# Kernel tuning notes

Measured on AMD Instinct MI355X. Metric: run time of the kernel, lower is better.

## Reference

```python
import jax, jax.numpy as jnp
import numpy as np

B, Cin, Cout, H, W = 4, 256, 256, 64, 64
DG, KH, KW = 2, 3, 3        # deformable_groups=2, kernel 3x3
K = KH * KW
CG = Cin // DG


def setup_inputs() -> dict:
    key = jax.random.key(0)
    ks = jax.random.split(key, 4)
    x = jax.random.normal(ks[0], (B, Cin, H, W), jnp.float32)
    # offset/mask-predicting 3x3 conv: 3*DG*K = 54 output channels
    # (small weights so sampled offsets stay in a realistic +-few-pixel range)
    w_off = jax.random.normal(ks[1], (3 * DG * K, Cin, KH, KW), jnp.float32) * 0.01
    b_off = jnp.zeros((3 * DG * K,), jnp.float32)
    weight = jax.random.normal(ks[2], (Cout, Cin, KH, KW), jnp.float32) * (1.0 / np.sqrt(Cin * K))
    bias = jnp.zeros((Cout,), jnp.float32)
    return {"x": x, "w_off": w_off, "b_off": b_off, "weight": weight, "bias": bias}


def _dcn_forward(x, w_off, b_off, weight, bias):
    # 1) predict offsets + modulation mask with a regular 3x3 conv
    om = jax.lax.conv_general_dilated(
        x, w_off, window_strides=(1, 1), padding=((1, 1), (1, 1)),
        dimension_numbers=('NCHW', 'OIHW', 'NCHW'))
    om = om + b_off[None, :, None, None]
    off = om[:, :2 * DG * K].reshape(B, DG, 2, K, H, W)        # [.,.,(dy,dx),k,h,w]
    mask = jax.nn.sigmoid(om[:, 2 * DG * K:]).reshape(B, DG, K, H, W)

    # 2) sampling positions: base grid (stride 1, pad 1, dilation 1) + learned offsets
    ky = jnp.repeat(jnp.arange(KH), KW).astype(jnp.float32)    # [K]
    kx = jnp.tile(jnp.arange(KW), KH).astype(jnp.float32)
    gy = jnp.arange(H, dtype=jnp.float32)
    gx = jnp.arange(W, dtype=jnp.float32)
    py = off[:, :, 0] + (gy[None, None, None, :, None] + ky[None, None, :, None, None] - 1.0)  # [B,DG,K,H,W]
    px = off[:, :, 1] + (gx[None, None, None, None, :] + kx[None, None, :, None, None] - 1.0)

    y0 = jnp.floor(py); x0 = jnp.floor(px)
    wy1 = py - y0; wx1 = px - x0
    wy0 = 1.0 - wy1; wx0 = 1.0 - wx1
    y0i = y0.astype(jnp.int32); x0i = x0.astype(jnp.int32)

    imgf = x.reshape(B, DG, CG, H * W)  # channel groups share their group's offsets

    def gather(iy, ix):
        # zero padding outside the image, as in the DCNv2 CUDA kernel
        valid = ((iy >= 0) & (iy < H) & (ix >= 0) & (ix < W)).astype(x.dtype)  # [B,DG,K,H,W]
        idx = jnp.clip(iy, 0, H - 1) * W + jnp.clip(ix, 0, W - 1)
        idx = idx.reshape(B, DG, K * H * W)
        v = jax.vmap(jax.vmap(lambda im, ii: im[:, ii]))(imgf, idx)  # [B,DG,CG,K*H*W]
        return v.reshape(B, DG, CG, K, H, W) * valid[:, :, None]

    # 3) bilinear interpolation of the 4 corners
    sampled = (gather(y0i,     x0i)     * (wy0 * wx0)[:, :, None]
             + gather(y0i,     x0i + 1) * (wy0 * wx1)[:, :, None]
             + gather(y0i + 1, x0i)     * (wy1 * wx0)[:, :, None]
             + gather(y0i + 1, x0i + 1) * (wy1 * wx1)[:, :, None])
    sampled = sampled * mask[:, :, None]  # modulation (DCNv2)

    # 4) weighted accumulation == grouped contraction over (channel, tap)
    wr = weight.reshape(Cout, DG, CG, K)
    out = jnp.einsum('odck,bdckhw->bohw', wr, sampled) + bias[None, :, None, None]
    return out


def reference(x, w_off, b_off, weight, bias):
    return _dcn_forward(x, w_off, b_off, weight, bias)
```

## Files before the change

### kernel.cpp

```cpp
#include <hip/hip_runtime.h>
#include <cstdint>

#define HW 4096

typedef __attribute__((ext_vector_type(8))) short bf16x8;
typedef __attribute__((ext_vector_type(4))) float f32x4;

__device__ __forceinline__ short f2bf(float f) {
    union { float f; uint32_t u; } v; v.f = f;
    uint32_t u = v.u;
    uint32_t r = (u + 0x7FFFu + ((u >> 16) & 1u)) >> 16;
    return (short)(r & 0xFFFFu);
}
__device__ __forceinline__ uint32_t cvtpk(float lo, float hi) {
    uint32_t r;
    asm("v_cvt_pk_bf16_f32 %0, %1, %2" : "=v"(r) : "v"(lo), "v"(hi));
    return r;
}
__device__ __forceinline__ float blo(uint32_t u) { return __uint_as_float(u << 16); }
__device__ __forceinline__ float bhi(uint32_t u) { return __uint_as_float(u & 0xFFFF0000u); }
__device__ __forceinline__ void glds16(const void* g, void* l) {
    __builtin_amdgcn_global_load_lds(
        (const __attribute__((address_space(1))) void*)g,
        (__attribute__((address_space(3))) void*)l, 16, 0, 0);
}

__global__ __launch_bounds__(256) void k_xt(
    const float* __restrict__ x, unsigned short* __restrict__ xT)
{
    __shared__ unsigned short s[64][65];
    const int t = threadIdx.x, lane = t & 63, grp = t >> 6;
    const int hw0 = blockIdx.x * 64, c0 = blockIdx.y * 64, b = blockIdx.z;
#pragma unroll
    for (int j = 0; j < 16; ++j) {
        int cc = grp * 16 + j;
        float v = x[((size_t)(b * 256 + c0 + cc)) * HW + hw0 + lane];
        s[cc][lane] = (unsigned short)f2bf(v);
    }
    __syncthreads();
#pragma unroll
    for (int j = 0; j < 16; ++j) {
        int hw2 = grp * 16 + j;
        xT[((size_t)b * HW + hw0 + hw2) * 256 + c0 + lane] = s[lane][hw2];
    }
}

__global__ __launch_bounds__(256) void k_wt2(
    const float* __restrict__ w_off, short* __restrict__ wTb)
{
    int e = blockIdx.x * 256 + threadIdx.x;
    int o = e / 2304, r = e - o * 2304;
    int tap = r >> 8, c = r & 255;
    wTb[e] = (o < 54) ? f2bf(w_off[(o * 256 + c) * 9 + tap]) : (short)0;
}

__global__ __launch_bounds__(256, 4) void k_omgemm(
    const short* __restrict__ wTb, const unsigned short* __restrict__ xT,
    float* __restrict__ om2p)
{
    __shared__ short As[2][64 * 32];
    __shared__ short Bs[2][64 * 32];
    const int t = threadIdx.x;
    const int wid = __builtin_amdgcn_readfirstlane(t >> 6);
    const int lane = t & 63, quad = lane >> 4, l16 = lane & 15;
    const int n0 = blockIdx.x * 64, b = n0 >> 12;
    const int ks = blockIdx.y;
    const int nr = t >> 2;
    const int ksh = (t & 3) * 8;
    const int px = (n0 + nr) & 4095, h = px >> 6, w = px & 63;
    const unsigned short* xb = xT + (size_t)b * HW * 256;
    const int cbase = ks * 18;

    auto loadB = [&](int c) -> uint4 {
        int tap = c >> 3, c0 = (c & 7) * 32;
        int hh = h + tap / 3 - 1, ww = w + tap % 3 - 1;
        uint4 bv = {0u, 0u, 0u, 0u};
        if (hh >= 0 && hh < 64 && ww >= 0 && ww < 64)
            bv = *(const uint4*)(xb + (size_t)(hh * 64 + ww) * 256 + c0 + ksh);
        return bv;
    };

    f32x4 acc[4];
#pragma unroll
    for (int i = 0; i < 4; ++i) acc[i] = (f32x4){0.f, 0.f, 0.f, 0.f};

    uint4 bv[2];
    bv[0] = loadB(cbase);
    glds16(wTb + (size_t)nr * 2304 + cbase * 32 + ksh, &As[0][t * 8]);
    *(uint4*)&Bs[0][t * 8] = bv[0];
    bv[1] = loadB(cbase + 1);

#pragma unroll 2
    for (int i = 0; i < 18; ++i) {
        const int p = i & 1;
        __syncthreads();
        if (i < 17) {
            glds16(wTb + (size_t)nr * 2304 + (cbase + i + 1) * 32 + ksh,
                   &As[1 - p][t * 8]);
            *(uint4*)&Bs[1 - p][t * 8] = bv[(i + 1) & 1];
        }
        if (i + 2 < 18) bv[i & 1] = loadB(cbase + i + 2);
        bf16x8 bf = *(const bf16x8*)&Bs[p][(wid * 16 + l16) * 32 + quad * 8];
#pragma unroll
        for (int mi = 0; mi < 4; ++mi) {
            bf16x8 af = *(const bf16x8*)&As[p][(mi * 16 + l16) * 32 + quad * 8];
            acc[mi] = __builtin_amdgcn_mfma_f32_16x16x32_bf16(af, bf, acc[mi], 0, 0, 0);
        }
    }
    const int n = n0 + wid * 16 + l16;
#pragma unroll
    for (int mi = 0; mi < 4; ++mi)
#pragma unroll
        for (int i = 0; i < 4; ++i)
            om2p[(size_t)(ks * 64 + mi * 16 + quad * 4 + i) * 16384 + n] = acc[mi][i];
}

__global__ __launch_bounds__(256) void k_wcvt2(
    const float* __restrict__ weight, short* __restrict__ a2)
{
    int e = blockIdx.x * 256 + threadIdx.x;
    int o = e / 2304, r = e - o * 2304;
    int dg = r / 1152, r2 = r - dg * 1152;
    int tap = r2 >> 7, c = r2 & 127;
    a2[e] = f2bf(weight[o * 2304 + (dg * 128 + c) * 9 + tap]);
}

__global__ __launch_bounds__(256) void k_plan(
    const float* __restrict__ om2p, const float* __restrict__ b_off,
    float4* __restrict__ planw, int4* __restrict__ plani)
{
    int e = blockIdx.x * 256 + threadIdx.x;
    int n = e & 16383, s = e >> 14;
    int dg = s >= 9 ? 1 : 0, tap = s - dg * 9;
    int h = (n >> 6) & 63, w = n & 63;
    int cdy = dg * 18 + tap, cdx = cdy + 9, cms = 36 + dg * 9 + tap;
    float dy = b_off[cdy], dx = b_off[cdx], ms = b_off[cms];
#pragma unroll
    for (int cs = 0; cs < 4; ++cs) {
        const float* p = om2p + (size_t)cs * 64 * 16384;
        dy += p[(size_t)cdy * 16384 + n];
        dx += p[(size_t)cdx * 16384 + n];
        ms += p[(size_t)cms * 16384 + n];
    }
    ms = 1.f / (1.f + __expf(-ms));
    float py = dy + (float)(h + tap / 3 - 1);
    float qx = dx + (float)(w + tap % 3 - 1);
    float y0f = floorf(py), x0f = floorf(qx);
    float wy1 = py - y0f, wx1 = qx - x0f;
    float wy0 = 1.f - wy1, wx0 = 1.f - wx1;
    int y0 = (int)y0f, x0 = (int)x0f;
    int y1 = y0 + 1, x1 = x0 + 1;
    bool vy0 = (y0 >= 0) & (y0 < 64), vy1 = (y1 >= 0) & (y1 < 64);
    bool vx0 = (x0 >= 0) & (x0 < 64), vx1 = (x1 >= 0) & (x1 < 64);
    int cy0 = min(max(y0, 0), 63), cy1 = min(max(y1, 0), 63);
    int cx0 = min(max(x0, 0), 63), cx1 = min(max(x1, 0), 63);
    float4 wv;
    wv.x = (vy0 && vx0) ? wy0 * wx0 * ms : 0.f;
    wv.y = (vy0 && vx1) ? wy0 * wx1 * ms : 0.f;
    wv.z = (vy1 && vx0) ? wy1 * wx0 * ms : 0.f;
    wv.w = (vy1 && vx1) ? wy1 * wx1 * ms : 0.f;
    int4 iv = make_int4((cy0 * 64 + cx0) << 9, (cy0 * 64 + cx1) << 9,
                        (cy1 * 64 + cx0) << 9, (cy1 * 64 + cx1) << 9);
    planw[e] = wv;
    plani[e] = iv;
}

__global__ __launch_bounds__(1024, 4) void k_fused(
    const short* __restrict__ A, const unsigned short* __restrict__ xT,
    const float4* __restrict__ planw, const int4* __restrict__ plani,
    const float* __restrict__ bias, float* __restrict__ out)
{
    __shared__ short As[2][4][256 * 32];
    __shared__ short Bs[2][4][64 * 32];
    const int t = threadIdx.x;
    const int wid = __builtin_amdgcn_readfirstlane(t >> 6);
    const int lane = t & 63;
    const int quad = lane >> 4, l16 = lane & 15;
    const int wr = wid & 7, wc = wid >> 3;

    const int lin = blockIdx.x;
    const int bn = ((lin & 7) << 5) | (lin >> 3);

    const int n0 = bn * 64, b = n0 >> 12;
    const char* xbb = (const char*)xT + (size_t)b * HW * 512;
    const int px = t >> 4;
    const int cc = (t >> 2) & 3;
    const int q8 = (t & 3) * 8;
    const int n = n0 + px;

    f32x4 acc[2][2];
#pragma unroll
    for (int i = 0; i < 2; ++i)
#pragma unroll
        for (int j = 0; j < 2; ++j) acc[i][j] = (f32x4){0.f, 0.f, 0.f, 0.f};

    float4 pw[2];
    int4 pi[2];
    uint4 g[2][4];

    auto planload = [&](int S) {
        pw[S & 1] = planw[(size_t)S * 16384 + n];
        pi[S & 1] = plani[(size_t)S * 16384 + n];
    };
    auto gather = [&](int j, uint4* gd) {
        const int cb = ((j >= 9 ? 128 : 0) + cc * 32 + q8) * 2;
        const int4 i4 = pi[j & 1];
        gd[0] = *(const uint4*)(xbb + i4.x + cb);
        gd[1] = *(const uint4*)(xbb + i4.y + cb);
        gd[2] = *(const uint4*)(xbb + i4.z + cb);
        gd[3] = *(const uint4*)(xbb + i4.w + cb);
    };
    const int arow = t >> 2;
    const int aq = t & 3;
    const int asw = (aq ^ ((arow >> 1) & 3)) * 8;
    auto stageA = [&](int j, int buf) {
#pragma unroll
        for (int ss = 0; ss < 4; ++ss)
            glds16(A + (size_t)arow * 2304 + (4 * j + ss) * 32 + asw,
                   &As[buf][ss][arow * 32 + aq * 8]);
    };
    const int bsw = ((t & 3) ^ ((px >> 1) & 3)) * 8;
    auto packwrite = [&](int j, int buf) {
        const float4 w4 = pw[j & 1];
        const uint4* gd = g[j & 1];
        float a0 = w4.x * blo(gd[0].x) + w4.y * blo(gd[1].x) + w4.z * blo(gd[2].x) + w4.w * blo(gd[3].x);
        float a1 = w4.x * bhi(gd[0].x) + w4.y * bhi(gd[1].x) + w4.z * bhi(gd[2].x) + w4.w * bhi(gd[3].x);
        float a2v = w4.x * blo(gd[0].y) + w4.y * blo(gd[1].y) + w4.z * blo(gd[2].y) + w4.w * blo(gd[3].y);
        float a3 = w4.x * bhi(gd[0].y) + w4.y * bhi(gd[1].y) + w4.z * bhi(gd[2].y) + w4.w * bhi(gd[3].y);
        float a4 = w4.x * blo(gd[0].z) + w4.y * blo(gd[1].z) + w4.z * blo(gd[2].z) + w4.w * blo(gd[3].z);
        float a5 = w4.x * bhi(gd[0].z) + w4.y * bhi(gd[1].z) + w4.z * bhi(gd[2].z) + w4.w * bhi(gd[3].z);
        float a6 = w4.x * blo(gd[0].w) + w4.y * blo(gd[1].w) + w4.z * blo(gd[2].w) + w4.w * blo(gd[3].w);
        float a7 = w4.x * bhi(gd[0].w) + w4.y * bhi(gd[1].w) + w4.z * bhi(gd[2].w) + w4.w * bhi(gd[3].w);
        uint4 o;
        o.x = cvtpk(a0, a1); o.y = cvtpk(a2v, a3);
        o.z = cvtpk(a4, a5); o.w = cvtpk(a6, a7);
        *(uint4*)&Bs[buf][cc][px * 32 + bsw] = o;
    };

    planload(0);
    gather(0, g[0]);
    stageA(0, 0);
    packwrite(0, 0);
    planload(1);
    gather(1, g[1]);

#pragma unroll 2
    for (int i = 0; i < 18; ++i) {
        const int p = i & 1;
        __syncthreads();
        if (i + 2 < 18) planload(i + 2);
        if (i < 17) {
            stageA(i + 1, 1 - p);
            packwrite(i + 1, 1 - p);
        }
        if (i + 2 < 18) gather(i + 2, g[i & 1]);
#pragma unroll
        for (int ss = 0; ss < 4; ++ss) {
            bf16x8 bfr[2];
#pragma unroll
            for (int ni = 0; ni < 2; ++ni) {
                const int row = wc * 32 + ni * 16 + l16;
                bfr[ni] = *(const bf16x8*)&Bs[p][ss][row * 32 + (quad ^ ((row >> 1) & 3)) * 8];
            }
#pragma unroll
            for (int mi = 0; mi < 2; ++mi) {
                const int row = wr * 32 + mi * 16 + l16;
                bf16x8 af = *(const bf16x8*)&As[p][ss][row * 32 + (quad ^ ((row >> 1) & 3)) * 8];
#pragma unroll
                for (int ni = 0; ni < 2; ++ni)
                    acc[mi][ni] = __builtin_amdgcn_mfma_f32_16x16x32_bf16(
                        af, bfr[ni], acc[mi][ni], 0, 0, 0);
            }
        }
    }

    const int m0 = wr * 32;
#pragma unroll
    for (int mi = 0; mi < 2; ++mi)
#pragma unroll
        for (int ni = 0; ni < 2; ++ni) {
            int nn = n0 + wc * 32 + ni * 16 + l16;
            int bidx = nn >> 12, hw = nn & 4095;
            float* op = out + (size_t)bidx * 256 * 4096 + hw;
#pragma unroll
            for (int r = 0; r < 4; ++r) {
                int m = m0 + mi * 16 + quad * 4 + r;
                op[(size_t)m * 4096] = acc[mi][ni][r] + bias[m];
            }
        }
}

extern "C" void kernel_launch(void* const* d_in, const int* in_sizes, int n_in,
                              void* d_out, int out_size, void* d_ws, size_t ws_size,
                              hipStream_t stream)
{
    const float* x      = (const float*)d_in[0];
    const float* w_off  = (const float*)d_in[1];
    const float* b_off  = (const float*)d_in[2];
    const float* weight = (const float*)d_in[3];
    const float* bias   = (const float*)d_in[4];
    float* out = (float*)d_out;
    char* ws = (char*)d_ws;

    unsigned short* xT   = (unsigned short*)(ws);
    short*          a2   = (short*)(ws + 8388608);
    short*          wTb  = (short*)(ws + 9568256);
    float4*         planw= (float4*)(ws + 9863168);
    int4*           plani= (int4*)(ws + 14581760);
    float*          om2p = (float*)d_out;

    hipLaunchKernelGGL(k_xt, dim3(64, 4, 4), dim3(256), 0, stream, x, xT);
    hipLaunchKernelGGL(k_wt2, dim3(576), dim3(256), 0, stream, w_off, wTb);
    hipLaunchKernelGGL(k_omgemm, dim3(256, 4), dim3(256), 0, stream, wTb, xT, om2p);
    hipLaunchKernelGGL(k_wcvt2, dim3(2304), dim3(256), 0, stream, weight, a2);
    hipLaunchKernelGGL(k_plan, dim3(1152), dim3(256), 0, stream, om2p, b_off, planw, plani);
    hipLaunchKernelGGL(k_fused, dim3(256), dim3(1024), 0, stream,
                       a2, xT, planw, plani, bias, out);
}
```

Measured before the change: 144.3 us.

## Merge weight conversion kernels and replace syncthreads with partial waitcnt barrier

Merges the two weight-conversion kernels into one launch, removing one kernel launch. In the fused gather-GEMM loop, __syncthreads is replaced by an explicit s_waitcnt vmcnt(4) plus s_barrier, with sched_barriers pinning the instruction order. Plan index loads are prefetched one stage further ahead, so gathers can stay in flight across the barrier. This relies on hand-counted outstanding memory operations, which is fragile: a wrong count gives a race.

After: 142.3 us. About the same (-1.4%).

```diff
diff --git a/kernel.cpp b/kernel.cpp
--- a/kernel.cpp
+++ b/kernel.cpp
@@ -45,13 +45,22 @@
     }
 }
 
-__global__ __launch_bounds__(256) void k_wt2(
-    const float* __restrict__ w_off, short* __restrict__ wTb)
+__global__ __launch_bounds__(256) void k_wcvt_all(
+    const float* __restrict__ weight, const float* __restrict__ w_off,
+    short* __restrict__ a2, short* __restrict__ wTb)
 {
     int e = blockIdx.x * 256 + threadIdx.x;
-    int o = e / 2304, r = e - o * 2304;
-    int tap = r >> 8, c = r & 255;
-    wTb[e] = (o < 54) ? f2bf(w_off[(o * 256 + c) * 9 + tap]) : (short)0;
+    if (e < 589824) {
+        int o = e / 2304, r = e - o * 2304;
+        int dg = r / 1152, r2 = r - dg * 1152;
+        int tap = r2 >> 7, c = r2 & 127;
+        a2[e] = f2bf(weight[o * 2304 + (dg * 128 + c) * 9 + tap]);
+    } else {
+        int e2 = e - 589824;
+        int o = e2 / 2304, r = e2 - o * 2304;
+        int tap = r >> 8, c = r & 255;
+        wTb[e2] = (o < 54) ? f2bf(w_off[(o * 256 + c) * 9 + tap]) : (short)0;
+    }
 }
 
 __global__ __launch_bounds__(256, 4) void k_omgemm(
@@ -113,16 +122,6 @@
 #pragma unroll
         for (int i = 0; i < 4; ++i)
             om2p[(size_t)(ks * 64 + mi * 16 + quad * 4 + i) * 16384 + n] = acc[mi][i];
-}
-
-__global__ __launch_bounds__(256) void k_wcvt2(
-    const float* __restrict__ weight, short* __restrict__ a2)
-{
-    int e = blockIdx.x * 256 + threadIdx.x;
-    int o = e / 2304, r = e - o * 2304;
-    int dg = r / 1152, r2 = r - dg * 1152;
-    int tap = r2 >> 7, c = r2 & 127;
-    a2[e] = f2bf(weight[o * 2304 + (dg * 128 + c) * 9 + tap]);
 }
 
 __global__ __launch_bounds__(256) void k_plan(
@@ -198,10 +197,8 @@
     int4 pi[2];
     uint4 g[2][4];
 
-    auto planload = [&](int S) {
-        pw[S & 1] = planw[(size_t)S * 16384 + n];
-        pi[S & 1] = plani[(size_t)S * 16384 + n];
-    };
+    auto pwload = [&](int S) { pw[S & 1] = planw[(size_t)S * 16384 + n]; };
+    auto piload = [&](int S) { pi[S & 1] = plani[(size_t)S * 16384 + n]; };
     auto gather = [&](int j, uint4* gd) {
         const int cb = ((j >= 9 ? 128 : 0) + cc * 32 + q8) * 2;
         const int4 i4 = pi[j & 1];
@@ -237,22 +234,34 @@
         *(uint4*)&Bs[buf][cc][px * 32 + bsw] = o;
     };
 
-    planload(0);
+    pwload(0);
+    piload(0);
     gather(0, g[0]);
     stageA(0, 0);
+    __builtin_amdgcn_sched_barrier(0);
     packwrite(0, 0);
-    planload(1);
+    pwload(1);
+    piload(1);
+    piload(2);
     gather(1, g[1]);
 
 #pragma unroll 2
     for (int i = 0; i < 18; ++i) {
         const int p = i & 1;
-        __syncthreads();
-        if (i + 2 < 18) planload(i + 2);
+        __builtin_amdgcn_sched_barrier(0);
+        if (i < 17)
+            asm volatile("s_waitcnt vmcnt(4) lgkmcnt(0)" ::: "memory");
+        else
+            asm volatile("s_waitcnt vmcnt(0) lgkmcnt(0)" ::: "memory");
+        __builtin_amdgcn_s_barrier();
+        __builtin_amdgcn_sched_barrier(0);
         if (i < 17) {
             stageA(i + 1, 1 - p);
+            __builtin_amdgcn_sched_barrier(0);
             packwrite(i + 1, 1 - p);
         }
+        if (i + 2 < 18) pwload(i + 2);
+        if (i + 3 < 18) piload(i + 3);
         if (i + 2 < 18) gather(i + 2, g[i & 1]);
 #pragma unroll
         for (int ss = 0; ss < 4; ++ss) {
@@ -310,9 +319,9 @@
     float*          om2p = (float*)d_out;
 
     hipLaunchKernelGGL(k_xt, dim3(64, 4, 4), dim3(256), 0, stream, x, xT);
-    hipLaunchKernelGGL(k_wt2, dim3(576), dim3(256), 0, stream, w_off, wTb);
+    hipLaunchKernelGGL(k_wcvt_all, dim3(2880), dim3(256), 0, stream,
+                       weight, w_off, a2, wTb);
     hipLaunchKernelGGL(k_omgemm, dim3(256, 4), dim3(256), 0, stream, wTb, xT, om2p);
-    hipLaunchKernelGGL(k_wcvt2, dim3(2304), dim3(256), 0, stream, weight, a2);
     hipLaunchKernelGGL(k_plan, dim3(1152), dim3(256), 0, stream, om2p, b_off, planw, plani);
     hipLaunchKernelGGL(k_fused, dim3(256), dim3(1024), 0, stream,
                        a2, xT, planw, plani, bias, out);
```
